# Kernel optimization log

Measured on AMD Instinct MI355X. Metric: run time of the kernel, lower is better.

## Reference

```python
import jax, jax.numpy as jnp
import numpy as np

ALPHA = 0.5  # distance-decay base (self.alpha)

def setup_inputs() -> dict:
    key = jax.random.key(0)
    N, E, D_IN, D_OUT = 50000, 800000, 128, 128
    k1, k2, k3, k4, k5 = jax.random.split(key, 5)
    h = jax.random.normal(k1, (N, D_IN), dtype=jnp.float32)
    # first N edges are self-loops so every node has in/out degree >= 1
    src = jnp.concatenate([jnp.arange(N), jax.random.randint(k2, (E - N,), 0, N)]).astype(jnp.int32)
    dst = jnp.concatenate([jnp.arange(N), jax.random.randint(k3, (E - N,), 0, N)]).astype(jnp.int32)
    distance = jax.random.randint(k4, (E,), 0, 6).astype(jnp.int32)
    limit = float(np.sqrt(6.0 / (D_IN + D_OUT)))  # xavier_uniform
    weight = jax.random.uniform(k5, (D_IN, D_OUT), jnp.float32, -limit, limit)
    bias = jnp.zeros((D_OUT,), jnp.float32)
    return {"h": h, "src": src, "dst": dst, "distance": distance, "weight": weight, "bias": bias}

def reference(h, src, dst, distance, weight, bias):
    N = h.shape[0]
    ones = jnp.ones(src.shape[0], jnp.float32)
    out_deg = jax.ops.segment_sum(ones, src, num_segments=N)  # [N]
    in_deg = jax.ops.segment_sum(ones, dst, num_segments=N)   # [N]
    # source-side symmetric norm
    feat = h * (out_deg ** -0.5)[:, None]                     # [N, D]
    # per-edge message: gathered src feature * alpha^distance
    w = jnp.power(jnp.float32(ALPHA), distance.astype(jnp.float32))  # [E]
    msg = feat[src] * w[:, None]                              # [E, D]
    # mean over mailbox == segment-sum / in-degree
    agg = jax.ops.segment_sum(msg, dst, num_segments=N) / in_deg[:, None]  # [N, D]
    rst = agg @ weight                                        # [N, D_OUT]
    rst = rst * (in_deg ** -0.5)[:, None] + bias
    return rst
```

## Files before the change

kernel.cpp:

```cpp
#include <hip/hip_runtime.h>


constexpr int D = 128;
constexpr int HC = 64;
constexpr int NWMAX = 25088;
constexpr int PNODES = 32;
constexpr int PCAP = 768;
constexpr int CHUNK = 8192;

typedef __attribute__((ext_vector_type(8))) short bf16x8;
typedef __attribute__((ext_vector_type(4))) float f32x4;

__device__ __forceinline__ float bf16_to_f(unsigned int u16) {
    union { unsigned int u; float f; } c; c.u = u16 << 16; return c.f;
}
__device__ __forceinline__ unsigned int f_to_bf16(float f) {
    union { float f; unsigned int u; } c; c.f = f;
    unsigned int u = c.u;
    u += 0x7fffu + ((u >> 16) & 1u);
    return u >> 16;
}

__global__ __launch_bounds__(256) void k_hist(const int* __restrict__ key,
        unsigned int* __restrict__ slices, int E, int NW, int chunk) {
    __shared__ unsigned int bins[NWMAX];
    for (int i = threadIdx.x; i < NW; i += 256) bins[i] = 0;
    __syncthreads();
    int c = blockIdx.x;
    int e0 = c * chunk, e1 = min(e0 + chunk, E);
    for (int i = e0 + threadIdx.x * 4; i < e1; i += 1024) {
        if (i + 3 < e1) {
            int4 k4 = *(const int4*)&key[i];
            atomicAdd(&bins[k4.x >> 1], 1u << ((k4.x & 1) * 16));
            atomicAdd(&bins[k4.y >> 1], 1u << ((k4.y & 1) * 16));
            atomicAdd(&bins[k4.z >> 1], 1u << ((k4.z & 1) * 16));
            atomicAdd(&bins[k4.w >> 1], 1u << ((k4.w & 1) * 16));
        } else {
            for (int e = i; e < e1; e++)
                atomicAdd(&bins[key[e] >> 1], 1u << ((key[e] & 1) * 16));
        }
    }
    __syncthreads();
    unsigned int* o = slices + (size_t)c * NW;
    for (int i = threadIdx.x; i < NW; i += 256) o[i] = bins[i];
}

__global__ __launch_bounds__(256) void k_scale_cast(const unsigned int* __restrict__ slices,
        const float4* __restrict__ h4, uint4* __restrict__ hs4,
        const float* __restrict__ W, unsigned short* __restrict__ Wt,
        int N, int NW, int wblk) {
    if (blockIdx.x == wblk) {
        for (int i = threadIdx.x; i < D * D; i += 256) {
            int k = i >> 7, n = i & 127;
            Wt[n * D + k] = (unsigned short)f_to_bf16(W[i]);
        }
        return;
    }
    __shared__ float osc[256];
    int n0 = blockIdx.x * 256;
    int n = n0 + threadIdx.x;
    if (n < N) {
        int wi = n >> 1, sh = (n & 1) * 16;
        unsigned int s = 0;
        #pragma unroll 8
        for (int c = 0; c < HC; c++) s += slices[(size_t)c * NW + wi];
        osc[threadIdx.x] = rsqrtf((float)((s >> sh) & 0xffffu));
    }
    __syncthreads();
    int grp = threadIdx.x >> 4, lane = threadIdx.x & 15;
    int rend = min(256, N - n0);
    for (int r = grp; r < rend; r += 16) {
        int row = n0 + r;
        float sc = osc[r];
        float4 a = h4[(size_t)row * 32 + lane * 2];
        float4 b = h4[(size_t)row * 32 + lane * 2 + 1];
        uint4 o;
        o.x = f_to_bf16(a.x * sc) | (f_to_bf16(a.y * sc) << 16);
        o.y = f_to_bf16(a.z * sc) | (f_to_bf16(a.w * sc) << 16);
        o.z = f_to_bf16(b.x * sc) | (f_to_bf16(b.y * sc) << 16);
        o.w = f_to_bf16(b.z * sc) | (f_to_bf16(b.w * sc) << 16);
        hs4[(size_t)row * 16 + lane] = o;
    }
}

__global__ __launch_bounds__(256) void k_partition(const int* __restrict__ src,
        const int* __restrict__ dst, const int* __restrict__ dist,
        int* __restrict__ gcur, unsigned int* __restrict__ gbuf, int E, int P) {
    __shared__ unsigned int sorted[CHUNK];
    __shared__ int gidx[CHUNK];
    extern __shared__ int dyn[];
    int* hist = dyn;
    int* start = dyn + P;
    int* lofs = dyn + 2 * P;
    int* base_g = dyn + 3 * P;
    __shared__ int wsum[4];

    int tid = threadIdx.x;
    int lane = tid & 63, w = tid >> 6;
    int e0 = blockIdx.x * CHUNK;
    int e1 = min(e0 + CHUNK, E);
    int ce = e1 - e0;

    for (int b = tid; b < P; b += 256) hist[b] = 0;
    __syncthreads();

    for (int i = e0 + tid * 4; i < e1; i += 1024) {
        if (i + 3 < e1) {
            int4 d4 = *(const int4*)&dst[i];
            atomicAdd(&hist[d4.x >> 5], 1);
            atomicAdd(&hist[d4.y >> 5], 1);
            atomicAdd(&hist[d4.z >> 5], 1);
            atomicAdd(&hist[d4.w >> 5], 1);
        } else {
            for (int e = i; e < e1; e++) atomicAdd(&hist[dst[e] >> 5], 1);
        }
    }
    __syncthreads();

    int loc[7];
    int s = 0;
    #pragma unroll
    for (int j = 0; j < 7; j++) {
        int b = tid * 7 + j;
        int v = (b < P) ? hist[b] : 0;
        loc[j] = s;
        s += v;
    }
    int x = s;
    #pragma unroll
    for (int off = 1; off < 64; off <<= 1) {
        int t = __shfl_up(x, off, 64);
        if (lane >= off) x += t;
    }
    if (lane == 63) wsum[w] = x;
    __syncthreads();
    int tbase = x - s;
    #pragma unroll
    for (int k = 0; k < 4; k++) if (k < w) tbase += wsum[k];
    #pragma unroll
    for (int j = 0; j < 7; j++) {
        int b = tid * 7 + j;
        if (b < P) {
            int st = tbase + loc[j];
            start[b] = st;
            lofs[b] = st;
            int cnt = hist[b];
            if (cnt) base_g[b] = atomicAdd(&gcur[b], cnt);
        }
    }
    __syncthreads();

    for (int i = e0 + tid * 4; i < e1; i += 1024) {
        if (i + 3 < e1) {
            int4 s4 = *(const int4*)&src[i];
            int4 d4 = *(const int4*)&dst[i];
            int4 q4 = *(const int4*)&dist[i];
            #pragma unroll
            for (int j = 0; j < 4; j++) {
                int sv = (&s4.x)[j], dv = (&d4.x)[j], qv = (&q4.x)[j];
                int p = dv >> 5;
                unsigned int wd = (unsigned)sv | ((unsigned)(dv & 31) << 16)
                                | ((unsigned)qv << 21);
                int pos = atomicAdd(&lofs[p], 1);
                sorted[pos] = wd;
                int rank = base_g[p] + (pos - start[p]);
                gidx[pos] = (rank < PCAP) ? p * PCAP + rank : -1;
            }
        } else {
            for (int e = i; e < e1; e++) {
                int sv = src[e], dv = dst[e], qv = dist[e];
                int p = dv >> 5;
                unsigned int wd = (unsigned)sv | ((unsigned)(dv & 31) << 16)
                                | ((unsigned)qv << 21);
                int pos = atomicAdd(&lofs[p], 1);
                sorted[pos] = wd;
                int rank = base_g[p] + (pos - start[p]);
                gidx[pos] = (rank < PCAP) ? p * PCAP + rank : -1;
            }
        }
    }
    __syncthreads();

    for (int i = tid; i < ce; i += 256) {
        int g = gidx[i];
        if (g >= 0) gbuf[g] = sorted[i];
    }
}

__global__ __launch_bounds__(256, 4) void k_pagg(const uint4* __restrict__ hs4,
        const unsigned int* __restrict__ gbuf, const int* __restrict__ gcur,
        const unsigned short* __restrict__ Wt, const float* __restrict__ bias,
        float* __restrict__ out, int N) {
    __shared__ unsigned int elist[PCAP];
    __shared__ unsigned int slist[PCAP];
    __shared__ int h2[PNODES], st2[PNODES], lo2[PNODES];
    __shared__ unsigned short As[PNODES * 136];
    int p = blockIdx.x;
    int tid = threadIdx.x;
    int cnt = min(gcur[p], PCAP);
    const unsigned int* gp = gbuf + (size_t)p * PCAP;

    if (tid < PNODES) h2[tid] = 0;
    __syncthreads();
    for (int i = tid; i < cnt; i += 256) {
        unsigned int wd = gp[i];
        elist[i] = wd;
        atomicAdd(&h2[(wd >> 16) & 31], 1);
    }
    __syncthreads();
    if (tid < 64) {
        int v = (tid < PNODES) ? h2[tid] : 0;
        int x = v;
        #pragma unroll
        for (int off = 1; off < 32; off <<= 1) {
            int t = __shfl_up(x, off, 64);
            if ((tid & 63) >= off) x += t;
        }
        if (tid < PNODES) { st2[tid] = x - v; lo2[tid] = x - v; }
    }
    __syncthreads();
    for (int i = tid; i < cnt; i += 256) {
        unsigned int wd = elist[i];
        int pos = atomicAdd(&lo2[(wd >> 16) & 31], 1);
        slist[pos] = wd;
    }
    __syncthreads();

    int wv = tid >> 6, l64 = tid & 63;
    int lane16 = l64 & 15, sub = l64 >> 4;
    #pragma unroll
    for (int k = 0; k < 8; k++) {
        int dl = wv * 8 + k;
        int node = p * PNODES + dl;
        int deg = h2[dl], b = st2[dl];
        float acc[8] = {0.f, 0.f, 0.f, 0.f, 0.f, 0.f, 0.f, 0.f};
        for (int eo = 0; eo < deg; eo += 16) {
            uint4 hv[4];
            float cc[4];
            #pragma unroll
            for (int j = 0; j < 4; j++) {
                int off = eo + j * 4 + sub;
                bool valid = off < deg;
                unsigned int wd = slist[b + (valid ? off : 0)];
                cc[j] = valid ? __uint_as_float((127u - ((wd >> 21) & 7u)) << 23)
                              : 0.f;
                hv[j] = hs4[(size_t)(wd & 0xffffu) * 16 + lane16];
            }
            #pragma unroll
            for (int j = 0; j < 4; j++) {
                float c = cc[j];
                acc[0] += c * bf16_to_f(hv[j].x & 0xffffu);
                acc[1] += c * bf16_to_f(hv[j].x >> 16);
                acc[2] += c * bf16_to_f(hv[j].y & 0xffffu);
                acc[3] += c * bf16_to_f(hv[j].y >> 16);
                acc[4] += c * bf16_to_f(hv[j].z & 0xffffu);
                acc[5] += c * bf16_to_f(hv[j].z >> 16);
                acc[6] += c * bf16_to_f(hv[j].w & 0xffffu);
                acc[7] += c * bf16_to_f(hv[j].w >> 16);
            }
        }
        #pragma unroll
        for (int j = 0; j < 8; j++) {
            acc[j] += __shfl_xor(acc[j], 16, 64);
            acc[j] += __shfl_xor(acc[j], 32, 64);
        }
        if (sub == 0) {
            uint4 o = make_uint4(0u, 0u, 0u, 0u);
            if (node < N) {
                float fd = (float)deg;
                float sc = rsqrtf(fd) / fd;
                o.x = f_to_bf16(acc[0] * sc) | (f_to_bf16(acc[1] * sc) << 16);
                o.y = f_to_bf16(acc[2] * sc) | (f_to_bf16(acc[3] * sc) << 16);
                o.z = f_to_bf16(acc[4] * sc) | (f_to_bf16(acc[5] * sc) << 16);
                o.w = f_to_bf16(acc[6] * sc) | (f_to_bf16(acc[7] * sc) << 16);
            }
            *(uint4*)&As[dl * 136 + lane16 * 8] = o;
        }
    }
    __syncthreads();

    int m = l64 & 15, quad = l64 >> 4;
    int mt = wv & 1, ntb = (wv >> 1) * 4;
    f32x4 acc2[4];
    #pragma unroll
    for (int t = 0; t < 4; t++) acc2[t] = (f32x4){0.f, 0.f, 0.f, 0.f};
    #pragma unroll
    for (int s = 0; s < 4; s++) {
        bf16x8 a = *(const bf16x8*)&As[(mt * 16 + m) * 136 + quad * 8 + s * 32];
        #pragma unroll
        for (int t = 0; t < 4; t++) {
            int n = (ntb + t) * 16 + m;
            bf16x8 b = *(const bf16x8*)&Wt[n * D + quad * 8 + s * 32];
            acc2[t] = __builtin_amdgcn_mfma_f32_16x16x32_bf16(a, b, acc2[t], 0, 0, 0);
        }
    }
    int orow0 = p * PNODES + mt * 16 + quad * 4;
    #pragma unroll
    for (int t = 0; t < 4; t++) {
        int n = (ntb + t) * 16 + m;
        float bz = bias[n];
        #pragma unroll
        for (int r = 0; r < 4; r++) {
            int grow = orow0 + r;
            if (grow < N) out[(size_t)grow * D + n] = acc2[t][r] + bz;
        }
    }
}

extern "C" void kernel_launch(void* const* d_in, const int* in_sizes, int n_in,
                              void* d_out, int out_size, void* d_ws, size_t ws_size,
                              hipStream_t stream) {
    const float* h    = (const float*)d_in[0];
    const int*   src  = (const int*)d_in[1];
    const int*   dst  = (const int*)d_in[2];
    const int*   dist = (const int*)d_in[3];
    const float* W    = (const float*)d_in[4];
    const float* bias = (const float*)d_in[5];
    float* out = (float*)d_out;
    const int N = in_sizes[0] / D;
    const int E = in_sizes[1];

    const int NW = (N + 1) / 2;
    const int hchunk = (((E + HC - 1) / HC) + 3) & ~3;
    const int P = (N + PNODES - 1) / PNODES;

    char* ws = (char*)d_ws;
    size_t p = 0;
    auto alloc = [&](size_t bytes) -> char* {
        char* r = ws + p;
        p = (p + bytes + 511) & ~(size_t)511;
        return r;
    };
    unsigned int* slices = (unsigned int*)alloc((size_t)HC * NW * 4);
    int* gcur = (int*)alloc((size_t)P * 4);
    unsigned int* gbuf = (unsigned int*)alloc((size_t)P * PCAP * 4);
    unsigned short* hs = (unsigned short*)alloc((size_t)N * D * 2);
    unsigned short* Wt = (unsigned short*)alloc((size_t)D * D * 2);

    hipMemsetAsync(gcur, 0, (size_t)P * 4, stream);
    k_hist<<<HC, 256, 0, stream>>>(src, slices, E, NW, hchunk);
    int nbsc = (N + 255) / 256;
    k_scale_cast<<<nbsc + 1, 256, 0, stream>>>(slices, (const float4*)h, (uint4*)hs,
                                               W, Wt, N, NW, nbsc);
    int nbA = (E + CHUNK - 1) / CHUNK;
    size_t dyn_sz = (size_t)4 * P * 4;
    k_partition<<<nbA, 256, dyn_sz, stream>>>(src, dst, dist, gcur, gbuf, E, P);
    k_pagg<<<P, 256, 0, stream>>>((const uint4*)hs, gbuf, gcur, Wt, bias, out, N);
}
```

Baseline: 178.5 us.

## Fuse source-degree histogram into partition kernel and raise aggregation occupancy

Merges the out-degree histogram and the edge-partition kernels into one launch, with extra blocks doing the histogram, so the two independent passes run concurrently and one launch is saved. Both roles share dynamic shared memory sized to the larger need, and the histogram chunk count drops from 64 to 32, which halves the slices the scale/cast kernel must reduce. The aggregation kernel's launch bounds are raised to 6 blocks per CU, which may force register spills. The larger uniform shared-memory allocation per block may lower occupancy for the partition blocks.

```diff
diff --git a/kernel.cpp b/kernel.cpp
--- a/kernel.cpp
+++ b/kernel.cpp
@@ -2,8 +2,7 @@
 
 
 constexpr int D = 128;
-constexpr int HC = 64;
-constexpr int NWMAX = 25088;
+constexpr int HC = 32;
 constexpr int PNODES = 32;
 constexpr int PCAP = 768;
 constexpr int CHUNK = 8192;
@@ -21,81 +20,46 @@
     return u >> 16;
 }
 
-__global__ __launch_bounds__(256) void k_hist(const int* __restrict__ key,
-        unsigned int* __restrict__ slices, int E, int NW, int chunk) {
-    __shared__ unsigned int bins[NWMAX];
-    for (int i = threadIdx.x; i < NW; i += 256) bins[i] = 0;
-    __syncthreads();
-    int c = blockIdx.x;
-    int e0 = c * chunk, e1 = min(e0 + chunk, E);
-    for (int i = e0 + threadIdx.x * 4; i < e1; i += 1024) {
-        if (i + 3 < e1) {
-            int4 k4 = *(const int4*)&key[i];
-            atomicAdd(&bins[k4.x >> 1], 1u << ((k4.x & 1) * 16));
-            atomicAdd(&bins[k4.y >> 1], 1u << ((k4.y & 1) * 16));
-            atomicAdd(&bins[k4.z >> 1], 1u << ((k4.z & 1) * 16));
-            atomicAdd(&bins[k4.w >> 1], 1u << ((k4.w & 1) * 16));
-        } else {
-            for (int e = i; e < e1; e++)
-                atomicAdd(&bins[key[e] >> 1], 1u << ((key[e] & 1) * 16));
-        }
-    }
-    __syncthreads();
-    unsigned int* o = slices + (size_t)c * NW;
-    for (int i = threadIdx.x; i < NW; i += 256) o[i] = bins[i];
-}
-
-__global__ __launch_bounds__(256) void k_scale_cast(const unsigned int* __restrict__ slices,
-        const float4* __restrict__ h4, uint4* __restrict__ hs4,
-        const float* __restrict__ W, unsigned short* __restrict__ Wt,
-        int N, int NW, int wblk) {
-    if (blockIdx.x == wblk) {
-        for (int i = threadIdx.x; i < D * D; i += 256) {
-            int k = i >> 7, n = i & 127;
-            Wt[n * D + k] = (unsigned short)f_to_bf16(W[i]);
-        }
+__global__ __launch_bounds__(256) void k_combo(const int* __restrict__ src,
+        const int* __restrict__ dst, const int* __restrict__ dist,
+        int* __restrict__ gcur, unsigned int* __restrict__ gbuf,
+        unsigned int* __restrict__ slices,
+        int E, int NW, int hchunk, int P, int nbA) {
+    extern __shared__ int dyn[];
+    int tid = threadIdx.x;
+
+    if (blockIdx.x >= nbA) {
+        unsigned int* bins = (unsigned int*)dyn;
+        for (int i = tid; i < NW; i += 256) bins[i] = 0;
+        __syncthreads();
+        int c = blockIdx.x - nbA;
+        int e0 = c * hchunk, e1 = min(e0 + hchunk, E);
+        for (int i = e0 + tid * 4; i < e1; i += 1024) {
+            if (i + 3 < e1) {
+                int4 k4 = *(const int4*)&src[i];
+                atomicAdd(&bins[k4.x >> 1], 1u << ((k4.x & 1) * 16));
+                atomicAdd(&bins[k4.y >> 1], 1u << ((k4.y & 1) * 16));
+                atomicAdd(&bins[k4.z >> 1], 1u << ((k4.z & 1) * 16));
+                atomicAdd(&bins[k4.w >> 1], 1u << ((k4.w & 1) * 16));
+            } else {
+                for (int e = i; e < e1; e++)
+                    atomicAdd(&bins[src[e] >> 1], 1u << ((src[e] & 1) * 16));
+            }
+        }
+        __syncthreads();
+        unsigned int* o = slices + (size_t)c * NW;
+        for (int i = tid; i < NW; i += 256) o[i] = bins[i];
         return;
     }
-    __shared__ float osc[256];
-    int n0 = blockIdx.x * 256;
-    int n = n0 + threadIdx.x;
-    if (n < N) {
-        int wi = n >> 1, sh = (n & 1) * 16;
-        unsigned int s = 0;
-        #pragma unroll 8
-        for (int c = 0; c < HC; c++) s += slices[(size_t)c * NW + wi];
-        osc[threadIdx.x] = rsqrtf((float)((s >> sh) & 0xffffu));
-    }
-    __syncthreads();
-    int grp = threadIdx.x >> 4, lane = threadIdx.x & 15;
-    int rend = min(256, N - n0);
-    for (int r = grp; r < rend; r += 16) {
-        int row = n0 + r;
-        float sc = osc[r];
-        float4 a = h4[(size_t)row * 32 + lane * 2];
-        float4 b = h4[(size_t)row * 32 + lane * 2 + 1];
-        uint4 o;
-        o.x = f_to_bf16(a.x * sc) | (f_to_bf16(a.y * sc) << 16);
-        o.y = f_to_bf16(a.z * sc) | (f_to_bf16(a.w * sc) << 16);
-        o.z = f_to_bf16(b.x * sc) | (f_to_bf16(b.y * sc) << 16);
-        o.w = f_to_bf16(b.z * sc) | (f_to_bf16(b.w * sc) << 16);
-        hs4[(size_t)row * 16 + lane] = o;
-    }
-}
-
-__global__ __launch_bounds__(256) void k_partition(const int* __restrict__ src,
-        const int* __restrict__ dst, const int* __restrict__ dist,
-        int* __restrict__ gcur, unsigned int* __restrict__ gbuf, int E, int P) {
-    __shared__ unsigned int sorted[CHUNK];
-    __shared__ int gidx[CHUNK];
-    extern __shared__ int dyn[];
-    int* hist = dyn;
-    int* start = dyn + P;
-    int* lofs = dyn + 2 * P;
-    int* base_g = dyn + 3 * P;
+
+    unsigned int* sorted = (unsigned int*)dyn;
+    int* gidx  = dyn + CHUNK;
+    int* hist  = dyn + 2 * CHUNK;
+    int* start = hist + P;
+    int* lofs  = start + P;
+    int* base_g = lofs + P;
     __shared__ int wsum[4];
 
-    int tid = threadIdx.x;
     int lane = tid & 63, w = tid >> 6;
     int e0 = blockIdx.x * CHUNK;
     int e1 = min(e0 + CHUNK, E);
@@ -187,7 +151,45 @@
     }
 }
 
-__global__ __launch_bounds__(256, 4) void k_pagg(const uint4* __restrict__ hs4,
+__global__ __launch_bounds__(256) void k_scale_cast(const unsigned int* __restrict__ slices,
+        const float4* __restrict__ h4, uint4* __restrict__ hs4,
+        const float* __restrict__ W, unsigned short* __restrict__ Wt,
+        int N, int NW, int wblk) {
+    if (blockIdx.x == wblk) {
+        for (int i = threadIdx.x; i < D * D; i += 256) {
+            int k = i >> 7, n = i & 127;
+            Wt[n * D + k] = (unsigned short)f_to_bf16(W[i]);
+        }
+        return;
+    }
+    __shared__ float osc[256];
+    int n0 = blockIdx.x * 256;
+    int n = n0 + threadIdx.x;
+    if (n < N) {
+        int wi = n >> 1, sh = (n & 1) * 16;
+        unsigned int s = 0;
+        #pragma unroll 8
+        for (int c = 0; c < HC; c++) s += slices[(size_t)c * NW + wi];
+        osc[threadIdx.x] = rsqrtf((float)((s >> sh) & 0xffffu));
+    }
+    __syncthreads();
+    int grp = threadIdx.x >> 4, lane = threadIdx.x & 15;
+    int rend = min(256, N - n0);
+    for (int r = grp; r < rend; r += 16) {
+        int row = n0 + r;
+        float sc = osc[r];
+        float4 a = h4[(size_t)row * 32 + lane * 2];
+        float4 b = h4[(size_t)row * 32 + lane * 2 + 1];
+        uint4 o;
+        o.x = f_to_bf16(a.x * sc) | (f_to_bf16(a.y * sc) << 16);
+        o.y = f_to_bf16(a.z * sc) | (f_to_bf16(a.w * sc) << 16);
+        o.z = f_to_bf16(b.x * sc) | (f_to_bf16(b.y * sc) << 16);
+        o.w = f_to_bf16(b.z * sc) | (f_to_bf16(b.w * sc) << 16);
+        hs4[(size_t)row * 16 + lane] = o;
+    }
+}
+
+__global__ __launch_bounds__(256, 6) void k_pagg(const uint4* __restrict__ hs4,
         const unsigned int* __restrict__ gbuf, const int* __restrict__ gcur,
         const unsigned short* __restrict__ Wt, const float* __restrict__ bias,
         float* __restrict__ out, int N) {
@@ -323,6 +325,7 @@
     const int NW = (N + 1) / 2;
     const int hchunk = (((E + HC - 1) / HC) + 3) & ~3;
     const int P = (N + PNODES - 1) / PNODES;
+    const int nbA = (E + CHUNK - 1) / CHUNK;
 
     char* ws = (char*)d_ws;
     size_t p = 0;
@@ -337,13 +340,15 @@
     unsigned short* hs = (unsigned short*)alloc((size_t)N * D * 2);
     unsigned short* Wt = (unsigned short*)alloc((size_t)D * D * 2);
 
+    size_t dyn_part = ((size_t)2 * CHUNK + 4 * P) * 4;
+    size_t dyn_hist = (size_t)NW * 4;
+    size_t dyn_sz = dyn_part > dyn_hist ? dyn_part : dyn_hist;
+
     hipMemsetAsync(gcur, 0, (size_t)P * 4, stream);
-    k_hist<<<HC, 256, 0, stream>>>(src, slices, E, NW, hchunk);
+    k_combo<<<nbA + HC, 256, dyn_sz, stream>>>(src, dst, dist, gcur, gbuf,
+                                               slices, E, NW, hchunk, P, nbA);
     int nbsc = (N + 255) / 256;
     k_scale_cast<<<nbsc + 1, 256, 0, stream>>>(slices, (const float4*)h, (uint4*)hs,
                                                W, Wt, N, NW, nbsc);
-    int nbA = (E + CHUNK - 1) / CHUNK;
-    size_t dyn_sz = (size_t)4 * P * 4;
-    k_partition<<<nbA, 256, dyn_sz, stream>>>(src, dst, dist, gcur, gbuf, E, P);
     k_pagg<<<P, 256, 0, stream>>>((const uint4*)hs, gbuf, gcur, Wt, bias, out, N);
 }
```

New measurement: 168.5 us. 1.06x faster.
